# Optimization experiments

Measured on AMD Instinct MI355X. Metric: run time of the kernel, lower is better.

The kernel has to match this reference:

```python
import jax, jax.numpy as jnp
import numpy as np

N_NODES = 100000


def setup_inputs() -> dict:
    key = jax.random.key(0)
    k1, k2, k3, k4, k5, k6 = jax.random.split(key, 6)
    N, E, F_IN, F_OUT = N_NODES, 1600000, 128, 128
    stdv = 1.0 / np.sqrt(F_OUT)
    return {
        "input_features": jax.random.normal(k1, (N, F_IN), dtype=jnp.float32),
        "edge_row": jnp.sort(jax.random.randint(k2, (E,), 0, N, dtype=jnp.int32)),
        "edge_col": jax.random.randint(k3, (E,), 0, N, dtype=jnp.int32),
        "edge_val": jax.random.uniform(k4, (E,), dtype=jnp.float32),
        "weight": jax.random.uniform(k5, (F_IN, F_OUT), minval=-stdv, maxval=stdv, dtype=jnp.float32),
        "bias": jax.random.uniform(k6, (F_OUT,), minval=-stdv, maxval=stdv, dtype=jnp.float32),
    }


def reference(input_features, edge_row, edge_col, edge_val, weight, bias):
    # support = X @ W   [N, F_out]  (dense GEMM)
    support = jnp.matmul(input_features, weight)
    # output = spmm(adj, support): COO adjacency, segment-sum over destination rows
    msgs = edge_val[:, None] * support[edge_col]          # [E, F_out] gather
    output = jax.ops.segment_sum(msgs, edge_row, num_segments=N_NODES)
    return output + bias
```

## Files before the change

### kernel.cpp

```cpp
#include <hip/hip_runtime.h>

typedef unsigned int uint;
typedef unsigned short ushort;
typedef __attribute__((ext_vector_type(4))) float f32x4;
typedef __attribute__((ext_vector_type(4))) uint u32x4;
typedef __attribute__((ext_vector_type(2))) uint u32x2;

#define NNODES 100000
#define NEDGES 1600000
#define FD 128
#define BM 64

__device__ __forceinline__ ushort f2bf(float f) {
    uint u = __float_as_uint(f);
    u += 0x7fffu + ((u >> 16) & 1u);
    return (ushort)(u >> 16);
}
__device__ __forceinline__ uint cvt_pk_bf16(float lo, float hi) {
    uint r;
    asm("v_cvt_pk_bf16_f32 %0, %1, %2" : "=v"(r) : "v"(lo), "v"(hi));
    return r;
}
__device__ __forceinline__ int swz(int row, int k) {
    return (row * 256 + k * 2) ^ ((row & 7) << 4);
}
__device__ __forceinline__ float bflo(uint s) { return __uint_as_float(s << 16); }
__device__ __forceinline__ float bfhi(uint s) { return __uint_as_float(s & 0xffff0000u); }

__global__ __launch_bounds__(256) void build_wt(const float* __restrict__ W,
                                                ushort* __restrict__ Wt) {
    const int sid = blockIdx.x * 256 + threadIdx.x;
    const int n = sid & 127, k0 = (sid >> 7) * 4;
    const float w0 = W[(k0 + 0) * FD + n];
    const float w1 = W[(k0 + 1) * FD + n];
    const float w2 = W[(k0 + 2) * FD + n];
    const float w3 = W[(k0 + 3) * FD + n];
    u32x2 p;
    p.x = cvt_pk_bf16(w0, w1);
    p.y = cvt_pk_bf16(w2, w3);
    *(u32x2*)((char*)Wt + swz(n, k0)) = p;
}

__global__ __launch_bounds__(256) void build_rowptr(const int* __restrict__ rows,
                                                    int* __restrict__ ptr) {
    const int r = blockIdx.x * 256 + threadIdx.x;
    if (r > NNODES) return;
    int lo = 0, hi = NEDGES;
    while (lo < hi) {
        const int mid = (lo + hi) >> 1;
        const bool lt = rows[mid] < r;
        lo = lt ? mid + 1 : lo;
        hi = lt ? hi : mid;
    }
    ptr[r] = lo;
}

__global__ __launch_bounds__(256) void gemm_mfma(const float* __restrict__ X,
                                                 const ushort* __restrict__ Wt,
                                                 ushort* __restrict__ S) {
    __shared__ ushort As[BM * FD];
    __shared__ ushort Bs[FD * FD];
    const int tid = threadIdx.x;
    const int row0 = blockIdx.x * BM;

    #pragma unroll
    for (int it = 0; it < 8; ++it) {
        const int idx = tid + it * 256;
        const int r = idx >> 5, k0 = (idx & 31) * 4;
        const int grow = min(row0 + r, NNODES - 1);
        const float4 g = *(const float4*)&X[grow * FD + k0];
        u32x2 p;
        p.x = cvt_pk_bf16(g.x, g.y);
        p.y = cvt_pk_bf16(g.z, g.w);
        *(u32x2*)((char*)As + swz(r, k0)) = p;
    }
    #pragma unroll
    for (int it = 0; it < 8; ++it) {
        const int b = (tid + it * 256) * 16;
        *(u32x4*)((char*)Bs + b) = *(const u32x4*)((const char*)Wt + b);
    }
    __syncthreads();

    const int lane = tid & 63, wv = tid >> 6;
    const int l15 = lane & 15, kg = lane >> 4;
    const int arow = wv * 16 + l15;

    f32x4 acc[8];
    #pragma unroll
    for (int i = 0; i < 8; ++i) acc[i] = (f32x4)0.f;

    #pragma unroll
    for (int ks = 0; ks < 4; ++ks) {
        const int k0 = ks * 32 + kg * 8;
        const u32x4 a = *(const u32x4*)((const char*)As + swz(arow, k0));
        #pragma unroll
        for (int nf = 0; nf < 8; ++nf) {
            const u32x4 b = *(const u32x4*)((const char*)Bs + swz(nf * 16 + l15, k0));
            asm volatile("v_mfma_f32_16x16x32_bf16 %0, %1, %2, %0"
                         : "+v"(acc[nf]) : "v"(a), "v"(b));
        }
    }
    asm volatile("s_nop 7\ns_nop 7\ns_nop 7");

    #pragma unroll
    for (int nf = 0; nf < 8; ++nf) {
        const int col = nf * 16 + l15;
        #pragma unroll
        for (int r = 0; r < 4; ++r) {
            const int grow = row0 + wv * 16 + kg * 4 + r;
            S[grow * FD + col] = f2bf(acc[nf][r]);
        }
    }
}

__global__ __launch_bounds__(256) void spmm_csr(const int* __restrict__ ptr,
                                                const int* __restrict__ cols,
                                                const float* __restrict__ vals,
                                                const ushort* __restrict__ S,
                                                const float* __restrict__ bias,
                                                float* __restrict__ out) {
    const int row = (blockIdx.x * 256 + threadIdx.x) >> 6;
    const int lane = threadIdx.x & 63;
    const int f = lane * 2;
    const int e0 = __builtin_amdgcn_readfirstlane(ptr[row]);
    const int e1 = __builtin_amdgcn_readfirstlane(ptr[row + 1]);

    float ax[4] = {0.f, 0.f, 0.f, 0.f};
    float ay[4] = {0.f, 0.f, 0.f, 0.f};

    int e = e0;
    for (; e + 8 <= e1; e += 8) {
        int c[8]; float v[8]; uint s[8];
        #pragma unroll
        for (int j = 0; j < 8; ++j) { c[j] = cols[e + j]; v[j] = vals[e + j]; }
        #pragma unroll
        for (int j = 0; j < 8; ++j) s[j] = *(const uint*)&S[c[j] * FD + f];
        #pragma unroll
        for (int j = 0; j < 8; ++j) {
            ax[j & 3] = fmaf(v[j], bflo(s[j]), ax[j & 3]);
            ay[j & 3] = fmaf(v[j], bfhi(s[j]), ay[j & 3]);
        }
    }
    for (; e < e1; ++e) {
        const int c = cols[e];
        const float v = vals[e];
        const uint s = *(const uint*)&S[c * FD + f];
        ax[0] = fmaf(v, bflo(s), ax[0]);
        ay[0] = fmaf(v, bfhi(s), ay[0]);
    }

    float2 o;
    o.x = ((ax[0] + ax[1]) + (ax[2] + ax[3])) + bias[f];
    o.y = ((ay[0] + ay[1]) + (ay[2] + ay[3])) + bias[f + 1];
    *(float2*)&out[row * FD + f] = o;
}

extern "C" void kernel_launch(void* const* d_in, const int* in_sizes, int n_in,
                              void* d_out, int out_size, void* d_ws, size_t ws_size,
                              hipStream_t stream) {
    const float* X    = (const float*)d_in[0];
    const int*   erow = (const int*)d_in[1];
    const int*   ecol = (const int*)d_in[2];
    const float* eval_= (const float*)d_in[3];
    const float* W    = (const float*)d_in[4];
    const float* bias = (const float*)d_in[5];
    float* out = (float*)d_out;

    ushort* S   = (ushort*)d_ws;
    ushort* Wt  = (ushort*)((char*)d_ws + 26u * 1024 * 1024);
    int*    rpt = (int*)((char*)d_ws + 28u * 1024 * 1024);

    build_wt<<<16, 256, 0, stream>>>(W, Wt);
    build_rowptr<<<(NNODES + 256) / 256, 256, 0, stream>>>(erow, rpt);
    gemm_mfma<<<(NNODES + BM - 1) / BM, 256, 0, stream>>>(X, Wt, S);
    spmm_csr<<<NNODES / 4, 256, 0, stream>>>(rpt, ecol, eval_, S, bias, out);
}
```

Before: 94.86 us.

## Store support in feature-chunked layout and split SpMM by feature chunk

The GEMM now writes its bf16 output as eight contiguous 16-column chunks instead of row-major 128-wide rows. The SpMM launches one block group per feature chunk, and each wave processes 8 edges in parallel across lane groups, then reduces with cross-lane shuffles. The aim is to shrink the working set per chunk so the random gathers hit cache better, and to parallelise across edges. The cost is reading edge indices and values eight times, doing smaller 32-byte gathers, and leaving more lanes idle in the shuffle and output stage.

```diff
diff --git a/kernel.cpp b/kernel.cpp
--- a/kernel.cpp
+++ b/kernel.cpp
@@ -7,9 +7,12 @@
 typedef __attribute__((ext_vector_type(2))) uint u32x2;
 
 #define NNODES 100000
+#define NPAD   100032
 #define NEDGES 1600000
 #define FD 128
 #define BM 64
+#define NCHUNK 8
+#define CHELEM (NPAD * 16)
 
 __device__ __forceinline__ ushort f2bf(float f) {
     uint u = __float_as_uint(f);
@@ -104,55 +107,67 @@
 
     #pragma unroll
     for (int nf = 0; nf < 8; ++nf) {
-        const int col = nf * 16 + l15;
         #pragma unroll
         for (int r = 0; r < 4; ++r) {
             const int grow = row0 + wv * 16 + kg * 4 + r;
-            S[grow * FD + col] = f2bf(acc[nf][r]);
+            S[nf * CHELEM + grow * 16 + l15] = f2bf(acc[nf][r]);
         }
     }
 }
 
-__global__ __launch_bounds__(256) void spmm_csr(const int* __restrict__ ptr,
-                                                const int* __restrict__ cols,
-                                                const float* __restrict__ vals,
-                                                const ushort* __restrict__ S,
-                                                const float* __restrict__ bias,
-                                                float* __restrict__ out) {
-    const int row = (blockIdx.x * 256 + threadIdx.x) >> 6;
+__global__ __launch_bounds__(256) void spmm_chunk(const int* __restrict__ ptr,
+                                                  const int* __restrict__ cols,
+                                                  const float* __restrict__ vals,
+                                                  const ushort* __restrict__ S,
+                                                  const float* __restrict__ bias,
+                                                  float* __restrict__ out) {
+    const int bx = blockIdx.x;
+    const int chunk = bx & 7;
+    const int row = (bx >> 3) * 4 + (threadIdx.x >> 6);
     const int lane = threadIdx.x & 63;
-    const int f = lane * 2;
-    const int e0 = __builtin_amdgcn_readfirstlane(ptr[row]);
-    const int e1 = __builtin_amdgcn_readfirstlane(ptr[row + 1]);
+    const int slot = lane >> 3;
+    const int fl = lane & 7;
 
-    float ax[4] = {0.f, 0.f, 0.f, 0.f};
-    float ay[4] = {0.f, 0.f, 0.f, 0.f};
+    const int e0 = ptr[row];
+    const int e1 = ptr[row + 1];
+    const ushort* __restrict__ Sc = S + (size_t)chunk * CHELEM;
 
-    int e = e0;
-    for (; e + 8 <= e1; e += 8) {
-        int c[8]; float v[8]; uint s[8];
-        #pragma unroll
-        for (int j = 0; j < 8; ++j) { c[j] = cols[e + j]; v[j] = vals[e + j]; }
-        #pragma unroll
-        for (int j = 0; j < 8; ++j) s[j] = *(const uint*)&S[c[j] * FD + f];
-        #pragma unroll
-        for (int j = 0; j < 8; ++j) {
-            ax[j & 3] = fmaf(v[j], bflo(s[j]), ax[j & 3]);
-            ay[j & 3] = fmaf(v[j], bfhi(s[j]), ay[j & 3]);
-        }
+    float ax = 0.f, ay = 0.f, bx2 = 0.f, by2 = 0.f;
+
+    for (int e = e0; e < e1; e += 16) {
+        int i0 = e + slot;
+        int i1 = e + 8 + slot;
+        const bool ok0 = i0 < e1, ok1 = i1 < e1;
+        i0 = min(i0, e1 - 1);
+        i1 = min(i1, e1 - 1);
+        const int c0 = cols[i0];
+        const int c1 = cols[i1];
+        const float v0 = ok0 ? vals[i0] : 0.f;
+        const float v1 = ok1 ? vals[i1] : 0.f;
+        const uint s0 = *(const uint*)&Sc[c0 * 16 + fl * 2];
+        const uint s1 = *(const uint*)&Sc[c1 * 16 + fl * 2];
+        ax  = fmaf(v0, bflo(s0), ax);
+        ay  = fmaf(v0, bfhi(s0), ay);
+        bx2 = fmaf(v1, bflo(s1), bx2);
+        by2 = fmaf(v1, bfhi(s1), by2);
     }
-    for (; e < e1; ++e) {
-        const int c = cols[e];
-        const float v = vals[e];
-        const uint s = *(const uint*)&S[c * FD + f];
-        ax[0] = fmaf(v, bflo(s), ax[0]);
-        ay[0] = fmaf(v, bfhi(s), ay[0]);
+    ax += bx2;
+    ay += by2;
+
+    #pragma unroll
+    for (int m = 8; m < 64; m <<= 1) {
+        ax += __shfl_xor(ax, m);
+        ay += __shfl_xor(ay, m);
     }
 
-    float2 o;
-    o.x = ((ax[0] + ax[1]) + (ax[2] + ax[3])) + bias[f];
-    o.y = ((ay[0] + ay[1]) + (ay[2] + ay[3])) + bias[f + 1];
-    *(float2*)&out[row * FD + f] = o;
+    if (lane < 8) {
+        const int f = chunk * 16 + fl * 2;
+        const float2 bi = *(const float2*)&bias[f];
+        float2 o;
+        o.x = ax + bi.x;
+        o.y = ay + bi.y;
+        *(float2*)&out[row * FD + f] = o;
+    }
 }
 
 extern "C" void kernel_launch(void* const* d_in, const int* in_sizes, int n_in,
@@ -172,6 +187,6 @@
 
     build_wt<<<16, 256, 0, stream>>>(W, Wt);
     build_rowptr<<<(NNODES + 256) / 256, 256, 0, stream>>>(erow, rpt);
-    gemm_mfma<<<(NNODES + BM - 1) / BM, 256, 0, stream>>>(X, Wt, S);
-    spmm_csr<<<NNODES / 4, 256, 0, stream>>>(rpt, ecol, eval_, S, bias, out);
+    gemm_mfma<<<NPAD / BM, 256, 0, stream>>>(X, Wt, S);
+    spmm_chunk<<<(NNODES / 4) * NCHUNK, 256, 0, stream>>>(rpt, ecol, eval_, S, bias, out);
 }
```

Result: slower. 248.0 us (+161.4%).

## Quantize GEMM output to per-row int8 and process eight rows per wave in SpMM

Applied to the files above, without the earlier changes.

The intermediate support matrix is now stored as unsigned 8-bit values with a per-row scale, halving the bytes gathered per edge compared to bf16. Edge values are pre-multiplied by the source-row scale in a new kernel, and the zero-point offset is corrected through a running sum of scaled values. SpMM now has each wave stream a contiguous edge range covering eight rows using vector loads, flushing on row changes and writing bias for empty rows. This adds an extra kernel pass over the edges and introduces int8 quantization error, which may exceed accuracy tolerance.

```diff
diff --git a/kernel.cpp b/kernel.cpp
--- a/kernel.cpp
+++ b/kernel.cpp
@@ -2,20 +2,18 @@
 
 typedef unsigned int uint;
 typedef unsigned short ushort;
+typedef unsigned char uchar;
 typedef __attribute__((ext_vector_type(4))) float f32x4;
 typedef __attribute__((ext_vector_type(4))) uint u32x4;
 typedef __attribute__((ext_vector_type(2))) uint u32x2;
 
 #define NNODES 100000
+#define NPAD   100032
 #define NEDGES 1600000
 #define FD 128
 #define BM 64
-
-__device__ __forceinline__ ushort f2bf(float f) {
-    uint u = __float_as_uint(f);
-    u += 0x7fffu + ((u >> 16) & 1u);
-    return (ushort)(u >> 16);
-}
+#define RPW 8
+
 __device__ __forceinline__ uint cvt_pk_bf16(float lo, float hi) {
     uint r;
     asm("v_cvt_pk_bf16_f32 %0, %1, %2" : "=v"(r) : "v"(lo), "v"(hi));
@@ -24,8 +22,6 @@
 __device__ __forceinline__ int swz(int row, int k) {
     return (row * 256 + k * 2) ^ ((row & 7) << 4);
 }
-__device__ __forceinline__ float bflo(uint s) { return __uint_as_float(s << 16); }
-__device__ __forceinline__ float bfhi(uint s) { return __uint_as_float(s & 0xffff0000u); }
 
 __global__ __launch_bounds__(256) void build_wt(const float* __restrict__ W,
                                                 ushort* __restrict__ Wt) {
@@ -55,9 +51,10 @@
     ptr[r] = lo;
 }
 
-__global__ __launch_bounds__(256) void gemm_mfma(const float* __restrict__ X,
-                                                 const ushort* __restrict__ Wt,
-                                                 ushort* __restrict__ S) {
+__global__ __launch_bounds__(256) void gemm_mfma_q8(const float* __restrict__ X,
+                                                    const ushort* __restrict__ Wt,
+                                                    uchar* __restrict__ S8,
+                                                    float* __restrict__ scale) {
     __shared__ ushort As[BM * FD];
     __shared__ ushort Bs[FD * FD];
     const int tid = threadIdx.x;
@@ -102,57 +99,123 @@
     }
     asm volatile("s_nop 7\ns_nop 7\ns_nop 7");
 
-    #pragma unroll
-    for (int nf = 0; nf < 8; ++nf) {
-        const int col = nf * 16 + l15;
+    __syncthreads();
+    uchar* As8 = (uchar*)As;
+
+    #pragma unroll
+    for (int r = 0; r < 4; ++r) {
+        float m = 0.f;
         #pragma unroll
-        for (int r = 0; r < 4; ++r) {
-            const int grow = row0 + wv * 16 + kg * 4 + r;
-            S[grow * FD + col] = f2bf(acc[nf][r]);
+        for (int nf = 0; nf < 8; ++nf) m = fmaxf(m, fabsf(acc[nf][r]));
+        m = fmaxf(m, __shfl_xor(m, 1));
+        m = fmaxf(m, __shfl_xor(m, 2));
+        m = fmaxf(m, __shfl_xor(m, 4));
+        m = fmaxf(m, __shfl_xor(m, 8));
+        m = fmaxf(m, 1e-20f);
+        const int lrow = wv * 16 + kg * 4 + r;
+        if (l15 == 0) scale[row0 + lrow] = m * (1.f / 127.f);
+        const float inv = 127.f / m;
+        #pragma unroll
+        for (int nf = 0; nf < 8; ++nf) {
+            const int q = (int)rintf(acc[nf][r] * inv) + 128;
+            As8[lrow * FD + nf * 16 + l15] = (uchar)q;
         }
     }
-}
-
-__global__ __launch_bounds__(256) void spmm_csr(const int* __restrict__ ptr,
-                                                const int* __restrict__ cols,
-                                                const float* __restrict__ vals,
-                                                const ushort* __restrict__ S,
-                                                const float* __restrict__ bias,
-                                                float* __restrict__ out) {
-    const int row = (blockIdx.x * 256 + threadIdx.x) >> 6;
+    __syncthreads();
+    #pragma unroll
+    for (int it = 0; it < 2; ++it) {
+        const int o = (tid + it * 256) * 16;
+        *(u32x4*)(S8 + (size_t)row0 * FD + o) = *(const u32x4*)(As8 + o);
+    }
+}
+
+__global__ __launch_bounds__(256) void build_vs(const int* __restrict__ ecol,
+                                                const float* __restrict__ eval_,
+                                                const float* __restrict__ scale,
+                                                float* __restrict__ VS) {
+    const int i = blockIdx.x * 256 + threadIdx.x;
+    if (i < NEDGES) VS[i] = eval_[i] * scale[ecol[i]];
+}
+
+__global__ __launch_bounds__(256) void spmm_q8(const int* __restrict__ rptr,
+                                               const int* __restrict__ erow,
+                                               const int* __restrict__ ecol,
+                                               const float* __restrict__ VS,
+                                               const uchar* __restrict__ S8,
+                                               const float* __restrict__ bias,
+                                               float* __restrict__ out) {
+    const int wv = (blockIdx.x * 256 + threadIdx.x) >> 6;
+    const int r0 = wv * RPW;
     const int lane = threadIdx.x & 63;
-    const int f = lane * 2;
-    const int e0 = __builtin_amdgcn_readfirstlane(ptr[row]);
-    const int e1 = __builtin_amdgcn_readfirstlane(ptr[row + 1]);
-
-    float ax[4] = {0.f, 0.f, 0.f, 0.f};
-    float ay[4] = {0.f, 0.f, 0.f, 0.f};
-
-    int e = e0;
-    for (; e + 8 <= e1; e += 8) {
-        int c[8]; float v[8]; uint s[8];
-        #pragma unroll
-        for (int j = 0; j < 8; ++j) { c[j] = cols[e + j]; v[j] = vals[e + j]; }
-        #pragma unroll
-        for (int j = 0; j < 8; ++j) s[j] = *(const uint*)&S[c[j] * FD + f];
-        #pragma unroll
-        for (int j = 0; j < 8; ++j) {
-            ax[j & 3] = fmaf(v[j], bflo(s[j]), ax[j & 3]);
-            ay[j & 3] = fmaf(v[j], bfhi(s[j]), ay[j & 3]);
+    const float2 b2 = *(const float2*)&bias[lane * 2];
+
+    const int E0 = __builtin_amdgcn_readfirstlane(rptr[r0]);
+    const int E1 = __builtin_amdgcn_readfirstlane(rptr[r0 + RPW]);
+
+    float a0 = 0.f, a1 = 0.f, sv = 0.f;
+    int rcur = __builtin_amdgcn_readfirstlane(E0 < E1 ? erow[E0] : 0);
+
+#define FLUSH() { float2 o;                                   \
+    o.x = fmaf(-128.f, sv, a0) + b2.x;                        \
+    o.y = fmaf(-128.f, sv, a1) + b2.y;                        \
+    *(float2*)&out[(size_t)rcur * FD + lane * 2] = o;         \
+    a0 = 0.f; a1 = 0.f; sv = 0.f; }
+
+    for (int eb = E0 & ~7; eb < E1; eb += 8) {
+        int4 ra, rb, ca, cb; float4 va, vb;
+        if (eb >= E0 && eb + 8 <= NEDGES) {
+            ra = *(const int4*)&erow[eb]; rb = *(const int4*)&erow[eb + 4];
+            ca = *(const int4*)&ecol[eb]; cb = *(const int4*)&ecol[eb + 4];
+            va = *(const float4*)&VS[eb]; vb = *(const float4*)&VS[eb + 4];
+        } else {
+#define LDM(F, i) { const int e = min(max(eb + i, 0), NEDGES - 1);            \
+            ((&F.x)[0]) = 0; }
+#undef LDM
+#define LDE(dst, i) { const int e = min(max(eb + (i), 0), NEDGES - 1);        \
+            dst = e; }
+            int e0_, e1_, e2_, e3_, e4_, e5_, e6_, e7_;
+            LDE(e0_, 0) LDE(e1_, 1) LDE(e2_, 2) LDE(e3_, 3)
+            LDE(e4_, 4) LDE(e5_, 5) LDE(e6_, 6) LDE(e7_, 7)
+            ra.x = erow[e0_]; ra.y = erow[e1_]; ra.z = erow[e2_]; ra.w = erow[e3_];
+            rb.x = erow[e4_]; rb.y = erow[e5_]; rb.z = erow[e6_]; rb.w = erow[e7_];
+            ca.x = ecol[e0_]; ca.y = ecol[e1_]; ca.z = ecol[e2_]; ca.w = ecol[e3_];
+            cb.x = ecol[e4_]; cb.y = ecol[e5_]; cb.z = ecol[e6_]; cb.w = ecol[e7_];
+            va.x = VS[e0_];   va.y = VS[e1_];   va.z = VS[e2_];   va.w = VS[e3_];
+            vb.x = VS[e4_];   vb.y = VS[e5_];   vb.z = VS[e6_];   vb.w = VS[e7_];
+#undef LDE
         }
-    }
-    for (; e < e1; ++e) {
-        const int c = cols[e];
-        const float v = vals[e];
-        const uint s = *(const uint*)&S[c * FD + f];
-        ax[0] = fmaf(v, bflo(s), ax[0]);
-        ay[0] = fmaf(v, bfhi(s), ay[0]);
-    }
-
-    float2 o;
-    o.x = ((ax[0] + ax[1]) + (ax[2] + ax[3])) + bias[f];
-    o.y = ((ay[0] + ay[1]) + (ay[2] + ay[3])) + bias[f + 1];
-    *(float2*)&out[row * FD + f] = o;
+#define GLD(c) (*(const ushort*)(S8 + ((uint)(c) << 7) + (lane << 1)))
+        const ushort g0 = GLD(ca.x); const ushort g1 = GLD(ca.y);
+        const ushort g2 = GLD(ca.z); const ushort g3 = GLD(ca.w);
+        const ushort g4 = GLD(cb.x); const ushort g5 = GLD(cb.y);
+        const ushort g6 = GLD(cb.z); const ushort g7 = GLD(cb.w);
+#undef GLD
+#define PROC(j, rj, vj, gj) {                                 \
+        const int e_ = eb + (j);                              \
+        if (e_ >= E0 && e_ < E1) {                            \
+            if (rj != rcur) { FLUSH(); rcur = rj; }           \
+            a0 = fmaf(vj, (float)(gj & 0xff), a0);            \
+            a1 = fmaf(vj, (float)(gj >> 8), a1);              \
+            sv += vj;                                         \
+        } }
+        PROC(0, ra.x, va.x, g0) PROC(1, ra.y, va.y, g1)
+        PROC(2, ra.z, va.z, g2) PROC(3, ra.w, va.w, g3)
+        PROC(4, rb.x, vb.x, g4) PROC(5, rb.y, vb.y, g5)
+        PROC(6, rb.z, vb.z, g6) PROC(7, rb.w, vb.w, g7)
+#undef PROC
+    }
+    if (E0 < E1) FLUSH();
+#undef FLUSH
+
+    const int rl = r0 + min(lane, RPW);
+    const int pa = rptr[rl], pb = rptr[min(rl + 1, NNODES)];
+    const unsigned long long mask =
+        __ballot(lane < RPW && pa == pb);
+    if (mask) {
+        for (int i = 0; i < RPW; ++i)
+            if ((mask >> i) & 1)
+                *(float2*)&out[(size_t)(r0 + i) * FD + lane * 2] = b2;
+    }
 }
 
 extern "C" void kernel_launch(void* const* d_in, const int* in_sizes, int n_in,
@@ -166,12 +229,15 @@
     const float* bias = (const float*)d_in[5];
     float* out = (float*)d_out;
 
-    ushort* S   = (ushort*)d_ws;
-    ushort* Wt  = (ushort*)((char*)d_ws + 26u * 1024 * 1024);
-    int*    rpt = (int*)((char*)d_ws + 28u * 1024 * 1024);
+    uchar* S8    = (uchar*)d_ws;
+    float* scale = (float*)((char*)d_ws + 13u * 1024 * 1024);
+    int*   rpt   = (int*)((char*)d_ws + 14u * 1024 * 1024);
+    float* VS    = (float*)((char*)d_ws + 15u * 1024 * 1024);
+    ushort* Wt   = (ushort*)((char*)d_ws + 22u * 1024 * 1024);
 
     build_wt<<<16, 256, 0, stream>>>(W, Wt);
     build_rowptr<<<(NNODES + 256) / 256, 256, 0, stream>>>(erow, rpt);
-    gemm_mfma<<<(NNODES + BM - 1) / BM, 256, 0, stream>>>(X, Wt, S);
-    spmm_csr<<<NNODES / 4, 256, 0, stream>>>(rpt, ecol, eval_, S, bias, out);
-}
+    gemm_mfma_q8<<<NPAD / BM, 256, 0, stream>>>(X, Wt, S8, scale);
+    build_vs<<<(NEDGES + 255) / 256, 256, 0, stream>>>(ecol, eval_, scale, VS);
+    spmm_q8<<<NNODES / RPW / 4, 256, 0, stream>>>(rpt, erow, ecol, VS, S8, bias, out);
+}
```

Result: slower. 123.8 us (+30.5%).
